# Kernel optimization log

Measured on AMD Instinct MI355X. Metric: run time of the kernel, lower is better.

Reference implementation:

```python
import jax, jax.numpy as jnp
import numpy as np
import math

B, T, Z, H, DOF = 256, 200, 64, 256, 12
NUM_LINKS = 13
POS_DIM = (NUM_LINKS + 1) * 3  # 42
TIME_BANDS = 6
TIME_DIM = 2 * TIME_BANDS + 1  # 13
ACTION_SCALE = 0.25
TRACK_ALPHA = 1.0
SIGMA_MIN, SIGMA_MAX = 0.05, 0.5


def setup_inputs() -> dict:
    key = jax.random.key(0)
    ks = iter(jax.random.split(key, 32))
    rn = lambda shape, s=0.1: jax.random.normal(next(ks), shape, jnp.float32) * s
    inp = {
        'z': jax.random.normal(next(ks), (B, Z), jnp.float32),
        'W_hz': rn((H, Z)), 'b_hz': rn((H,)),
        'W_cz': rn((H, Z)), 'b_cz': rn((H,)),
        'Wih': rn((4 * H, DOF + Z + TIME_DIM)), 'Whh': rn((4 * H, H)),
        'bih': rn((4 * H,)), 'bhh': rn((4 * H,)),
        'Wp1': rn((H, H)), 'bp1': rn((H,)),
        'Wp2': rn((DOF, H)), 'bp2': rn((DOF,)),
        'Wo1': rn((H, H)), 'bo1': rn((H,)),
        'Wo2': rn((3, H)), 'bo2': rn((3,)),
        'Wv': rn((POS_DIM, H)), 'bv': rn((POS_DIM,)),
        'Wfk': rn((NUM_LINKS * 3, DOF)), 'bfk': rn((NUM_LINKS * 3,)),
        'pos_mean': jax.random.normal(next(ks), (NUM_LINKS + 1, 3), jnp.float32),
        'pos_std': 0.5 + jax.random.uniform(next(ks), (NUM_LINKS + 1, 3), jnp.float32),
        'joint_lower': -jnp.ones((DOF,), jnp.float32),
        'joint_upper': jnp.ones((DOF,), jnp.float32),
        'default_dof_pos': jnp.zeros((DOF,), jnp.float32),
    }
    return inp


def _time_features():
    t = jnp.linspace(0.0, 1.0, T)
    feats = [t]
    for k in range(TIME_BANDS):
        f = 2.0 ** k
        feats.append(jnp.sin(2 * math.pi * f * t))
        feats.append(jnp.cos(2 * math.pi * f * t))
    return jnp.stack(feats, axis=-1)  # [T, TIME_DIM]


def reference(z, W_hz, b_hz, W_cz, b_cz, Wih, Whh, bih, bhh,
              Wp1, bp1, Wp2, bp2, Wo1, bo1, Wo2, bo2, Wv, bv, Wfk, bfk,
              pos_mean, pos_std, joint_lower, joint_upper, default_dof_pos):
    joint_range = (joint_upper - joint_lower) / 2.0
    joint_mean = (joint_upper + joint_lower) / 2.0
    time_feats = _time_features()  # [T, TIME_DIM]

    h0 = z @ W_hz.T + b_hz  # [B,H]
    c0 = z @ W_cz.T + b_cz
    prev0 = jnp.broadcast_to(default_dof_pos, (B, DOF))

    def step(carry, tf):
        h, c, prev = carry
        prev_norm = (prev - joint_mean) / joint_range
        x = jnp.concatenate([prev_norm, z, jnp.broadcast_to(tf, (B, TIME_DIM))], axis=-1)
        g = x @ Wih.T + bih + h @ Whh.T + bhh  # [B,4H]
        i, f, gg, o = jnp.split(g, 4, axis=-1)
        c_new = jax.nn.sigmoid(f) * c + jax.nn.sigmoid(i) * jnp.tanh(gg)
        h_new = jax.nn.sigmoid(o) * jnp.tanh(c_new)
        action = jnp.tanh(jax.nn.relu(h_new @ Wp1.T + bp1) @ Wp2.T + bp2)
        target = action * ACTION_SCALE + default_dof_pos
        cur = prev + TRACK_ALPHA * (target - prev)
        clamped = jnp.clip(cur, joint_lower, joint_upper)
        cur_in = cur + jax.lax.stop_gradient(clamped - cur)  # straight-through clamp
        obj = jax.nn.relu(h_new @ Wo1.T + bo1) @ Wo2.T + bo2
        return (h_new, c_new, jax.lax.stop_gradient(cur_in)), (h_new, action, cur, obj)

    _, (H_seq, actions, joints, objs) = jax.lax.scan(step, (h0, c0, prev0), time_feats)
    # [T,B,*] -> [B,T,*]
    H_seq = jnp.swapaxes(H_seq, 0, 1)
    actions_seq = jnp.swapaxes(actions, 0, 1)
    joint_traj = jnp.swapaxes(joints, 0, 1)
    object_traj = jnp.swapaxes(objs, 0, 1)

    agent_traj = joint_traj @ Wfk.T + bfk  # FK: [B,T,39]
    combined = jnp.concatenate([agent_traj, object_traj], axis=-1)  # [B,T,42]
    combined_rs = combined.reshape(B, T, NUM_LINKS + 1, 3)
    graph_x_mu = ((combined_rs - pos_mean) / pos_std).reshape(B, T, POS_DIM)

    sigma = SIGMA_MIN + (SIGMA_MAX - SIGMA_MIN) * jax.nn.sigmoid(H_seq @ Wv.T + bv)
    log_sigma_pos = jnp.log(sigma)
    return (graph_x_mu, joint_traj, actions_seq, log_sigma_pos)
```

## Files before the change

### kernel.cpp

```cpp
#include <hip/hip_runtime.h>
#include <math.h>

#define B_ 256
#define T_ 200
#define H_ 256
#define DOF_ 12

typedef __bf16 bf16;
typedef __bf16 bf16x8 __attribute__((ext_vector_type(8)));
typedef float f32x4 __attribute__((ext_vector_type(4)));

#define XK 288
#define XPAD 296
#define P1PAD 264

#define PI_D 3.14159265358979323846

#define OFF_TF     0u
#define OFF_TCONP  10400u
#define OFF_ZCP    829600u
#define OFF_H0     1878176u
#define OFF_C0     2140320u
#define OFF_WCOMB  2402464u
#define OFF_WP1    2992288u
#define OFF_WP2    3123360u
#define OFF_WO1    3131552u
#define OFF_WO2    3262624u
#define OFF_WV     3270816u
#define OFF_FLAGS  (OFF_WV + 21504u)
#define OFF_HX     3295392u
#define OFF_HSEQ   3558400u

__device__ __forceinline__ float sigf(float x) { return 1.f / (1.f + __expf(-x)); }
__device__ __forceinline__ float tanh_f(float x) {
  float a = fabsf(x);
  float e = __expf(-2.f * a);
  float t = (1.f - e) / (1.f + e);
  return x < 0.f ? -t : t;
}

#define LBAR() asm volatile("s_waitcnt lgkmcnt(0)\n\ts_barrier" ::: "memory")

__global__ void k_zflags(unsigned int* flags) {
  int i = threadIdx.x;
  if (i < 256)
    __hip_atomic_store(&flags[i], 0u, __ATOMIC_RELAXED, __HIP_MEMORY_SCOPE_AGENT);
}

__global__ void k_tfeat(float* tf) {
  int i = blockIdx.x * blockDim.x + threadIdx.x;
  if (i >= T_ * 13) return;
  int t = i / 13, j = i % 13;
  float tv = (float)t / 199.f;
  float v;
  if (j == 0) v = tv;
  else {
    int k = (j - 1) >> 1;
    float f = (float)(1 << k);
    double arg = 2.0 * PI_D * (double)f * (double)tv;
    v = (j & 1) ? (float)sin(arg) : (float)cos(arg);
  }
  tf[i] = v;
}

__global__ void k_prep(const float* __restrict__ tf, const float* __restrict__ Wih,
                       const float* __restrict__ z,
                       const float* __restrict__ bih, const float* __restrict__ bhh,
                       const float* __restrict__ Whz, const float* __restrict__ bhz,
                       const float* __restrict__ Wcz, const float* __restrict__ bcz,
                       float* tconp, float* zcp, float* h0, float* c0) {
  int i = blockIdx.x * blockDim.x + threadIdx.x;
  if (i < 204800) {
    int g = i & 3, q = i >> 2;
    int m = q & 127, hm = (q >> 7) & 1, t = q >> 8;
    int n = g * 256 + 128 * hm + m;
    float s = 0.f;
    #pragma unroll
    for (int j = 0; j < 13; ++j) s += tf[t * 13 + j] * Wih[n * 89 + 76 + j];
    tconp[i] = s;
    return;
  }
  i -= 204800;
  if (i < 262144) {
    int r = i & 3, g = (i >> 2) & 3, tid = (i >> 4) & 511;
    int half = (i >> 13) & 1, pairk = i >> 14;
    int wv = tid >> 6, lr = tid & 15, lq = (tid >> 4) & 3;
    int b = pairk * 16 + lq * 4 + r;
    int n = g * 256 + 128 * half + 16 * wv + lr;
    float s = bih[n] + bhh[n];
    for (int k = 0; k < 64; ++k) s += z[b * 64 + k] * Wih[n * 89 + 12 + k];
    zcp[i] = s;
    return;
  }
  i -= 262144;
  if (i < 65536) {
    int b = i / 256, u = i % 256;
    float s = bhz[u];
    for (int k = 0; k < 64; ++k) s += z[b * 64 + k] * Whz[u * 64 + k];
    h0[i] = s;
    return;
  }
  i -= 65536;
  if (i < 65536) {
    int b = i / 256, u = i % 256;
    float s = bcz[u];
    for (int k = 0; k < 64; ++k) s += z[b * 64 + k] * Wcz[u * 64 + k];
    c0[i] = s;
  }
}

__global__ void k_cast(const float* __restrict__ Whh, const float* __restrict__ Wih,
                       const float* __restrict__ Wp1, const float* __restrict__ Wp2,
                       const float* __restrict__ Wo1, const float* __restrict__ Wo2,
                       const float* __restrict__ Wv,
                       bf16* Wcomb, bf16* Wp1b, bf16* Wp2b, bf16* Wo1b,
                       bf16* Wo2b, bf16* Wvb) {
  int i = blockIdx.x * blockDim.x + threadIdx.x;
  if (i < 294912) {
    int n = i / XK, k = i % XK;
    float v = (k < 256) ? Whh[n * 256 + k]
            : ((k < 268) ? Wih[n * 89 + (k - 256)] : 0.f);
    Wcomb[i] = (bf16)v;
    return;
  }
  i -= 294912;
  if (i < 65536) { Wp1b[i] = (bf16)Wp1[i]; return; }
  i -= 65536;
  if (i < 4096) { int r = i / 256; Wp2b[i] = (bf16)((r < 12) ? Wp2[i] : 0.f); return; }
  i -= 4096;
  if (i < 65536) { Wo1b[i] = (bf16)Wo1[i]; return; }
  i -= 65536;
  if (i < 4096) { int r = i / 256; Wo2b[i] = (bf16)((r < 3) ? Wo2[i] : 0.f); return; }
  i -= 4096;
  if (i < 12288) { int r = i / 256; Wvb[i] = (bf16)((r < 42) ? Wv[i] : 0.f); }
}

__global__ __launch_bounds__(512)
__attribute__((amdgpu_waves_per_eu(2, 2))) void k_recur(
    const float* __restrict__ zcp, const float* __restrict__ tconp,
    const float* __restrict__ h0, const float* __restrict__ c0,
    const bf16* __restrict__ Wcomb, const bf16* __restrict__ Wp1b,
    const bf16* __restrict__ Wp2b,
    const float* __restrict__ bp1, const float* __restrict__ bp2,
    const float* __restrict__ jlo, const float* __restrict__ jhi,
    const float* __restrict__ ddp,
    unsigned long long* hx, unsigned int* flags,
    bf16* __restrict__ Hseq, float* __restrict__ outJ, float* __restrict__ outA) {
  __shared__ bf16 xbuf[16][XPAD];
  __shared__ bf16 w1[272][P1PAD];
  __shared__ bf16 p1buf[16][P1PAD];
  const int tid = threadIdx.x;
  const int wv = tid >> 6, ln = tid & 63, lr = ln & 15, lq = ln >> 4;
  const int bid = blockIdx.x;
  const int pairk = ((bid >> 4) << 3) | (bid & 7);
  const int half = (bid >> 3) & 1;
  const int lbid = pairk * 2 + half;
  const int pbid = bid ^ 8;
  const int b0 = pairk * 16;
  const int u_loc = 16 * wv + lr;
  const int u_gl = 128 * half + u_loc;

  for (int i = tid; i < 272 * 32; i += 512) {
    int r = i >> 5, c8 = (i & 31) * 8;
    bf16x8 v = (r < 256)
      ? *reinterpret_cast<const bf16x8*>(&Wp1b[r * 256 + c8])
      : *reinterpret_cast<const bf16x8*>(&Wp2b[(r - 256) * 256 + c8]);
    *reinterpret_cast<bf16x8*>(&w1[r][c8]) = v;
  }
  for (int i = tid; i < 16 * XPAD; i += 512) {
    int r = i / XPAD, c = i % XPAD;
    float v = 0.f;
    if (c < 256) v = h0[(b0 + r) * 256 + c];
    else if (c < 268) {
      int d = c - 256;
      float lo = jlo[d], hi = jhi[d];
      v = (ddp[d] - 0.5f * (hi + lo)) / (0.5f * (hi - lo));
    }
    xbuf[r][c] = (bf16)v;
  }

  bf16x8 wc[4][9];
  #pragma unroll
  for (int g = 0; g < 4; ++g)
    #pragma unroll
    for (int kt = 0; kt < 9; ++kt) {
      wc[g][kt] = *reinterpret_cast<const bf16x8*>(
          &Wcomb[(size_t)(g * 256 + u_gl) * XK + kt * 32 + lq * 8]);
      f32x4 tmp = __builtin_bit_cast(f32x4, wc[g][kt]);
      asm volatile("" : "+v"(tmp));
      wc[g][kt] = __builtin_bit_cast(bf16x8, tmp);
    }

  float c_reg[4];
  #pragma unroll
  for (int r = 0; r < 4; ++r) c_reg[r] = c0[(b0 + lq * 4 + r) * 256 + u_gl];
  f32x4 zcreg[4];
  #pragma unroll
  for (int g = 0; g < 4; ++g)
    zcreg[g] = *reinterpret_cast<const f32x4*>(
        zcp + ((size_t)lbid * 512 + tid) * 16 + g * 4);
  const float* tcb = tconp + (size_t)(half * 512 + u_loc * 4);
  const float bp1r0 = bp1[32 * wv + lr];
  const float bp1r1 = bp1[32 * wv + 16 + lr];
  float bp2r = 0.f, ddr = 0.f, lor = -1.f, hir = 1.f;
  if (lr < 12) { bp2r = bp2[lr]; ddr = ddp[lr]; lor = jlo[lr]; hir = jhi[lr]; }
  const float jmr = 0.5f * (hir + lor), jrr = 0.5f * (hir - lor);
  bf16* hs = Hseq + ((size_t)(b0 + lq * 4) * T_) * 256 + u_gl;

  unsigned int* myf = &flags[bid * 8 + wv];
  unsigned int* pf  = &flags[pbid * 8 + wv];
  const int wru = 16 * wv + (ln >> 2), wrc = ln & 3;
  const int rcol = 128 * (half ^ 1) + wru;
  unsigned long long* hxw0 = &hx[(((size_t)(pairk * 2 + 0) * 2 + half) * 128 + u_loc) * 4 + lq];
  unsigned long long* hxw1 = &hx[(((size_t)(pairk * 2 + 1) * 2 + half) * 128 + u_loc) * 4 + lq];
  unsigned long long* hxr0 = &hx[(((size_t)(pairk * 2 + 0) * 2 + (half ^ 1)) * 128 + wru) * 4 + wrc];
  unsigned long long* hxr1 = &hx[(((size_t)(pairk * 2 + 1) * 2 + (half ^ 1)) * 128 + wru) * 4 + wrc];

  f32x4 tcv = *reinterpret_cast<const f32x4*>(tcb);
  __syncthreads();
  bool dead = false;

  for (int t = 0; t < T_; ++t) {
    f32x4 ac[4];
    #pragma unroll
    for (int g = 0; g < 4; ++g) ac[g] = zcreg[g] + tcv[g];
    #pragma unroll
    for (int kt = 0; kt < 9; ++kt) {
      bf16x8 a = *reinterpret_cast<const bf16x8*>(&xbuf[lr][kt * 32 + lq * 8]);
      #pragma unroll
      for (int g = 0; g < 4; ++g)
        ac[g] = __builtin_amdgcn_mfma_f32_16x16x32_bf16(a, wc[g][kt], ac[g], 0, 0, 0);
    }
    LBAR();

    union { unsigned long long v; unsigned short s[4]; } pk;
    bf16 hb4[4];
    #pragma unroll
    for (int r = 0; r < 4; ++r) {
      float cn = sigf(ac[1][r]) * c_reg[r] + sigf(ac[0][r]) * tanh_f(ac[2][r]);
      float hn = sigf(ac[3][r]) * tanh_f(cn);
      c_reg[r] = cn;
      bf16 hb = (bf16)hn;
      hb4[r] = hb;
      xbuf[lq * 4 + r][u_gl] = hb;
      pk.s[r] = __builtin_bit_cast(unsigned short, hb);
    }
    __hip_atomic_store((t & 1) ? hxw1 : hxw0, pk.v,
                       __ATOMIC_RELAXED, __HIP_MEMORY_SCOPE_AGENT);
    asm volatile("s_waitcnt vmcnt(0)" ::: "memory");
    const unsigned int want = t + 1;
    if (ln == 0)
      __hip_atomic_store(myf, want, __ATOMIC_RELAXED, __HIP_MEMORY_SCOPE_AGENT);
    #pragma unroll
    for (int r = 0; r < 4; ++r)
      hs[(size_t)r * (T_ * 256) + (size_t)t * 256] = hb4[r];
    f32x4 tcn = *reinterpret_cast<const f32x4*>(
        tcb + (size_t)((t + 1 < T_) ? t + 1 : t) * 1024);

    if (!dead) {
      int guard = 1 << 18;
      for (;;) {
        unsigned int fv =
            __hip_atomic_load(pf, __ATOMIC_RELAXED, __HIP_MEMORY_SCOPE_AGENT);
        if ((int)(fv - want) >= 0) break;
        if (--guard == 0) { dead = true; break; }
      }
    }
    unsigned long long pv = __hip_atomic_load((t & 1) ? hxr1 : hxr0,
                                              __ATOMIC_RELAXED,
                                              __HIP_MEMORY_SCOPE_AGENT);
    {
      unsigned short* ph = (unsigned short*)&pv;
      #pragma unroll
      for (int j = 0; j < 4; ++j)
        xbuf[wrc * 4 + j][rcol] = __builtin_bit_cast(bf16, ph[j]);
    }
    LBAR();

    {
      f32x4 acc0 = {bp1r0, bp1r0, bp1r0, bp1r0};
      f32x4 acc1 = {bp1r1, bp1r1, bp1r1, bp1r1};
      #pragma unroll
      for (int kt = 0; kt < 8; ++kt) {
        bf16x8 av = *reinterpret_cast<const bf16x8*>(&xbuf[lr][kt * 32 + lq * 8]);
        bf16x8 b0v = *reinterpret_cast<const bf16x8*>(&w1[32 * wv + lr][kt * 32 + lq * 8]);
        bf16x8 b1v = *reinterpret_cast<const bf16x8*>(&w1[32 * wv + 16 + lr][kt * 32 + lq * 8]);
        acc0 = __builtin_amdgcn_mfma_f32_16x16x32_bf16(av, b0v, acc0, 0, 0, 0);
        acc1 = __builtin_amdgcn_mfma_f32_16x16x32_bf16(av, b1v, acc1, 0, 0, 0);
      }
      #pragma unroll
      for (int r = 0; r < 4; ++r) {
        p1buf[lq * 4 + r][32 * wv + lr] = (bf16)fmaxf(acc0[r], 0.f);
        p1buf[lq * 4 + r][32 * wv + 16 + lr] = (bf16)fmaxf(acc1[r], 0.f);
      }
    }
    LBAR();

    if (wv == 0) {
      f32x4 acc = {0.f, 0.f, 0.f, 0.f};
      #pragma unroll
      for (int kt = 0; kt < 8; ++kt) {
        bf16x8 ap = *reinterpret_cast<const bf16x8*>(&p1buf[lr][kt * 32 + lq * 8]);
        bf16x8 w2 = *reinterpret_cast<const bf16x8*>(&w1[256 + lr][kt * 32 + lq * 8]);
        acc = __builtin_amdgcn_mfma_f32_16x16x32_bf16(ap, w2, acc, 0, 0, 0);
      }
      if (lr < 12) {
        #pragma unroll
        for (int r = 0; r < 4; ++r) {
          int b = lq * 4 + r;
          float act = tanh_f(acc[r] + bp2r);
          float curp = act * 0.25f + ddr;
          float cl = fminf(fmaxf(curp, lor), hir);
          if (half == 0) {
            size_t o = ((size_t)(b0 + b) * T_ + t) * 12 + lr;
            outA[o] = act;
            outJ[o] = curp;
          }
          xbuf[b][256 + lr] = (bf16)((cl - jmr) / jrr);
        }
      }
    }
    LBAR();
    tcv = tcn;
  }
}

__global__ __launch_bounds__(256) void k_post(
    const bf16* __restrict__ Hseq, const bf16* __restrict__ Wo1b,
    const bf16* __restrict__ Wo2b, const bf16* __restrict__ Wvb,
    const float* __restrict__ bo1, const float* __restrict__ bo2,
    const float* __restrict__ bv,
    const float* __restrict__ Wfk, const float* __restrict__ bfk,
    const float* __restrict__ pm, const float* __restrict__ ps,
    const float* __restrict__ joints, float* __restrict__ out0,
    float* __restrict__ out3) {
  __shared__ bf16 u1buf[16][P1PAD];
  __shared__ float objbuf[16][3];
  __shared__ float jbuf[16][12];
  const int tid = threadIdx.x;
  const int wv = tid >> 6;
  const int ln = tid & 63;
  const int lr = ln & 15;
  const int lq = ln >> 4;

  bf16x8 wo1f[4][8];
  float bo1r[4];
  #pragma unroll
  for (int jn = 0; jn < 4; ++jn) {
    int n0 = wv * 64 + jn * 16;
    bo1r[jn] = bo1[n0 + lr];
    #pragma unroll
    for (int kt = 0; kt < 8; ++kt)
      wo1f[jn][kt] = *reinterpret_cast<const bf16x8*>(
          &Wo1b[(size_t)(n0 + lr) * 256 + kt * 32 + lq * 8]);
  }
  const int col = (wv - 1) * 16 + lr;
  bf16x8 wvf[8];
  float bvr = 0.f;
  if (wv >= 1) {
    #pragma unroll
    for (int kt = 0; kt < 8; ++kt)
      wvf[kt] = *reinterpret_cast<const bf16x8*>(
          &Wvb[(size_t)col * 256 + kt * 32 + lq * 8]);
    bvr = (col < 42) ? bv[col] : 0.f;
  }
  bf16x8 wo2f[8];
  if (wv == 0) {
    #pragma unroll
    for (int kt = 0; kt < 8; ++kt)
      wo2f[kt] = *reinterpret_cast<const bf16x8*>(
          &Wo2b[(size_t)lr * 256 + kt * 32 + lq * 8]);
  }

  for (int it = 0; it < 10; ++it) {
    int tt = blockIdx.x * 10 + it;
    size_t r0 = (size_t)tt * 16;
    bf16x8 ah[8];
    #pragma unroll
    for (int kt = 0; kt < 8; ++kt)
      ah[kt] = *reinterpret_cast<const bf16x8*>(&Hseq[(r0 + lr) * 256 + kt * 32 + lq * 8]);
    #pragma unroll
    for (int jn = 0; jn < 4; ++jn) {
      int n0 = wv * 64 + jn * 16;
      float bb = bo1r[jn];
      f32x4 acc = {bb, bb, bb, bb};
      #pragma unroll
      for (int kt = 0; kt < 8; ++kt)
        acc = __builtin_amdgcn_mfma_f32_16x16x32_bf16(ah[kt], wo1f[jn][kt], acc, 0, 0, 0);
      #pragma unroll
      for (int r = 0; r < 4; ++r)
        u1buf[lq * 4 + r][n0 + lr] = (bf16)fmaxf(acc[r], 0.f);
    }
    if (wv >= 1) {
      f32x4 acc = {bvr, bvr, bvr, bvr};
      #pragma unroll
      for (int kt = 0; kt < 8; ++kt)
        acc = __builtin_amdgcn_mfma_f32_16x16x32_bf16(ah[kt], wvf[kt], acc, 0, 0, 0);
      if (col < 42) {
        #pragma unroll
        for (int r = 0; r < 4; ++r) {
          float s = 0.05f + 0.45f * sigf(acc[r]);
          out3[(r0 + lq * 4 + r) * 42 + col] = __logf(s);
        }
      }
    }
    if (tid < 192) {
      int rr = tid / 12, d = tid % 12;
      jbuf[rr][d] = joints[(r0 + rr) * 12 + d];
    }
    __syncthreads();
    if (wv == 0) {
      bf16x8 ap[8];
      #pragma unroll
      for (int kt = 0; kt < 8; ++kt)
        ap[kt] = *reinterpret_cast<const bf16x8*>(&u1buf[lr][kt * 32 + lq * 8]);
      f32x4 acc = {0.f, 0.f, 0.f, 0.f};
      #pragma unroll
      for (int kt = 0; kt < 8; ++kt)
        acc = __builtin_amdgcn_mfma_f32_16x16x32_bf16(ap[kt], wo2f[kt], acc, 0, 0, 0);
      if (lr < 3) {
        #pragma unroll
        for (int r = 0; r < 4; ++r)
          objbuf[lq * 4 + r][lr] = acc[r] + bo2[lr];
      }
    }
    __syncthreads();
    for (int e = tid; e < 16 * 42; e += 256) {
      int rr = e / 42, pd = e % 42;
      float v;
      if (pd < 39) {
        float s = bfk[pd];
        #pragma unroll
        for (int d = 0; d < 12; ++d) s += jbuf[rr][d] * Wfk[pd * 12 + d];
        v = s;
      } else v = objbuf[rr][pd - 39];
      out0[(r0 + rr) * 42 + pd] = (v - pm[pd]) / ps[pd];
    }
    __syncthreads();
  }
}

extern "C" void kernel_launch(void* const* d_in, const int* in_sizes, int n_in,
                              void* d_out, int out_size, void* d_ws, size_t ws_size,
                              hipStream_t stream) {
  const float* z   = (const float*)d_in[0];
  const float* Whz = (const float*)d_in[1];
  const float* bhz = (const float*)d_in[2];
  const float* Wcz = (const float*)d_in[3];
  const float* bcz = (const float*)d_in[4];
  const float* Wih = (const float*)d_in[5];
  const float* Whh = (const float*)d_in[6];
  const float* bih = (const float*)d_in[7];
  const float* bhh = (const float*)d_in[8];
  const float* Wp1 = (const float*)d_in[9];
  const float* bp1 = (const float*)d_in[10];
  const float* Wp2 = (const float*)d_in[11];
  const float* bp2 = (const float*)d_in[12];
  const float* Wo1 = (const float*)d_in[13];
  const float* bo1 = (const float*)d_in[14];
  const float* Wo2 = (const float*)d_in[15];
  const float* bo2 = (const float*)d_in[16];
  const float* Wv  = (const float*)d_in[17];
  const float* bv  = (const float*)d_in[18];
  const float* Wfk = (const float*)d_in[19];
  const float* bfk = (const float*)d_in[20];
  const float* pm  = (const float*)d_in[21];
  const float* ps  = (const float*)d_in[22];
  const float* jlo = (const float*)d_in[23];
  const float* jhi = (const float*)d_in[24];
  const float* ddp = (const float*)d_in[25];

  char* ws = (char*)d_ws;
  float* tf    = (float*)(ws + OFF_TF);
  float* tconp = (float*)(ws + OFF_TCONP);
  float* zcp   = (float*)(ws + OFF_ZCP);
  float* h0    = (float*)(ws + OFF_H0);
  float* c0    = (float*)(ws + OFF_C0);
  bf16* Wcomb  = (bf16*)(ws + OFF_WCOMB);
  bf16* Wp1b   = (bf16*)(ws + OFF_WP1);
  bf16* Wp2b   = (bf16*)(ws + OFF_WP2);
  bf16* Wo1b   = (bf16*)(ws + OFF_WO1);
  bf16* Wo2b   = (bf16*)(ws + OFF_WO2);
  bf16* Wvb    = (bf16*)(ws + OFF_WV);
  unsigned long long* hx = (unsigned long long*)(ws + OFF_HX);
  unsigned int* flags    = (unsigned int*)(ws + OFF_FLAGS);
  bf16* Hseq   = (bf16*)(ws + OFF_HSEQ);

  float* out  = (float*)d_out;
  float* out0 = out;
  float* outJ = out + 2150400;
  float* outA = out + 2764800;
  float* out3 = out + 3379200;

  k_zflags<<<1, 256, 0, stream>>>(flags);
  k_tfeat<<<11, 256, 0, stream>>>(tf);
  k_prep<<<2336, 256, 0, stream>>>(tf, Wih, z, bih, bhh, Whz, bhz, Wcz, bcz,
                                   tconp, zcp, h0, c0);
  k_cast<<<1744, 256, 0, stream>>>(Whh, Wih, Wp1, Wp2, Wo1, Wo2, Wv,
                                   Wcomb, Wp1b, Wp2b, Wo1b, Wo2b, Wvb);
  k_recur<<<32, 512, 0, stream>>>(zcp, tconp, h0, c0, Wcomb, Wp1b, Wp2b,
                                  bp1, bp2, jlo, jhi, ddp, hx, flags,
                                  Hseq, outJ, outA);
  k_post<<<320, 256, 0, stream>>>(Hseq, Wo1b, Wo2b, Wvb, bo1, bo2, bv,
                                  Wfk, bfk, pm, ps, outJ, out0, out3);
}
```

Baseline: 1.122 ms.

## Replace flag-based cross-block handoff with sequence-tagged hidden-state packets

New measurement: 1.119 ms. Within noise of the previous version (-0.3%).

```diff
diff --git a/kernel.cpp b/kernel.cpp
--- a/kernel.cpp
+++ b/kernel.cpp
@@ -9,6 +9,7 @@
 typedef __bf16 bf16;
 typedef __bf16 bf16x8 __attribute__((ext_vector_type(8)));
 typedef float f32x4 __attribute__((ext_vector_type(4)));
+typedef unsigned long long u64;
 
 #define XK 288
 #define XPAD 296
@@ -27,9 +28,8 @@
 #define OFF_WO1    3131552u
 #define OFF_WO2    3262624u
 #define OFF_WV     3270816u
-#define OFF_FLAGS  (OFF_WV + 21504u)
 #define OFF_HX     3295392u
-#define OFF_HSEQ   3558400u
+#define OFF_HSEQ   3819680u
 
 __device__ __forceinline__ float sigf(float x) { return 1.f / (1.f + __expf(-x)); }
 __device__ __forceinline__ float tanh_f(float x) {
@@ -40,12 +40,6 @@
 }
 
 #define LBAR() asm volatile("s_waitcnt lgkmcnt(0)\n\ts_barrier" ::: "memory")
-
-__global__ void k_zflags(unsigned int* flags) {
-  int i = threadIdx.x;
-  if (i < 256)
-    __hip_atomic_store(&flags[i], 0u, __ATOMIC_RELAXED, __HIP_MEMORY_SCOPE_AGENT);
-}
 
 __global__ void k_tfeat(float* tf) {
   int i = blockIdx.x * blockDim.x + threadIdx.x;
@@ -135,8 +129,7 @@
   if (i < 12288) { int r = i / 256; Wvb[i] = (bf16)((r < 42) ? Wv[i] : 0.f); }
 }
 
-__global__ __launch_bounds__(512)
-__attribute__((amdgpu_waves_per_eu(2, 2))) void k_recur(
+__global__ __launch_bounds__(512, 2) void k_recur(
     const float* __restrict__ zcp, const float* __restrict__ tconp,
     const float* __restrict__ h0, const float* __restrict__ c0,
     const bf16* __restrict__ Wcomb, const bf16* __restrict__ Wp1b,
@@ -144,7 +137,7 @@
     const float* __restrict__ bp1, const float* __restrict__ bp2,
     const float* __restrict__ jlo, const float* __restrict__ jhi,
     const float* __restrict__ ddp,
-    unsigned long long* hx, unsigned int* flags,
+    u64* hxt,
     bf16* __restrict__ Hseq, float* __restrict__ outJ, float* __restrict__ outA) {
   __shared__ bf16 xbuf[16][XPAD];
   __shared__ bf16 w1[272][P1PAD];
@@ -155,7 +148,6 @@
   const int pairk = ((bid >> 4) << 3) | (bid & 7);
   const int half = (bid >> 3) & 1;
   const int lbid = pairk * 2 + half;
-  const int pbid = bid ^ 8;
   const int b0 = pairk * 16;
   const int u_loc = 16 * wv + lr;
   const int u_gl = 128 * half + u_loc;
@@ -179,17 +171,15 @@
     xbuf[r][c] = (bf16)v;
   }
 
-  bf16x8 wc[4][9];
+  f32x4 wc0[9], wc1[9], wc2[9], wc3[9];
   #pragma unroll
-  for (int g = 0; g < 4; ++g)
-    #pragma unroll
-    for (int kt = 0; kt < 9; ++kt) {
-      wc[g][kt] = *reinterpret_cast<const bf16x8*>(
-          &Wcomb[(size_t)(g * 256 + u_gl) * XK + kt * 32 + lq * 8]);
-      f32x4 tmp = __builtin_bit_cast(f32x4, wc[g][kt]);
-      asm volatile("" : "+v"(tmp));
-      wc[g][kt] = __builtin_bit_cast(bf16x8, tmp);
-    }
+  for (int kt = 0; kt < 9; ++kt) {
+    wc0[kt] = *reinterpret_cast<const f32x4*>(&Wcomb[(size_t)(0 * 256 + u_gl) * XK + kt * 32 + lq * 8]);
+    wc1[kt] = *reinterpret_cast<const f32x4*>(&Wcomb[(size_t)(1 * 256 + u_gl) * XK + kt * 32 + lq * 8]);
+    wc2[kt] = *reinterpret_cast<const f32x4*>(&Wcomb[(size_t)(2 * 256 + u_gl) * XK + kt * 32 + lq * 8]);
+    wc3[kt] = *reinterpret_cast<const f32x4*>(&Wcomb[(size_t)(3 * 256 + u_gl) * XK + kt * 32 + lq * 8]);
+    asm volatile("" : "+a"(wc0[kt]), "+a"(wc1[kt]), "+a"(wc2[kt]), "+a"(wc3[kt]));
+  }
 
   float c_reg[4];
   #pragma unroll
@@ -207,14 +197,12 @@
   const float jmr = 0.5f * (hir + lor), jrr = 0.5f * (hir - lor);
   bf16* hs = Hseq + ((size_t)(b0 + lq * 4) * T_) * 256 + u_gl;
 
-  unsigned int* myf = &flags[bid * 8 + wv];
-  unsigned int* pf  = &flags[pbid * 8 + wv];
   const int wru = 16 * wv + (ln >> 2), wrc = ln & 3;
   const int rcol = 128 * (half ^ 1) + wru;
-  unsigned long long* hxw0 = &hx[(((size_t)(pairk * 2 + 0) * 2 + half) * 128 + u_loc) * 4 + lq];
-  unsigned long long* hxw1 = &hx[(((size_t)(pairk * 2 + 1) * 2 + half) * 128 + u_loc) * 4 + lq];
-  unsigned long long* hxr0 = &hx[(((size_t)(pairk * 2 + 0) * 2 + (half ^ 1)) * 128 + wru) * 4 + wrc];
-  unsigned long long* hxr1 = &hx[(((size_t)(pairk * 2 + 1) * 2 + (half ^ 1)) * 128 + wru) * 4 + wrc];
+  u64* pws0 = hxt + ((((size_t)(pairk * 2 + 0) * 2 + half) * 128 + u_loc) * 4 + lq) * 2;
+  u64* pws1 = hxt + ((((size_t)(pairk * 2 + 1) * 2 + half) * 128 + u_loc) * 4 + lq) * 2;
+  u64* prs0 = hxt + ((((size_t)(pairk * 2 + 0) * 2 + (half ^ 1)) * 128 + wru) * 4 + wrc) * 2;
+  u64* prs1 = hxt + ((((size_t)(pairk * 2 + 1) * 2 + (half ^ 1)) * 128 + wru) * 4 + wrc) * 2;
 
   f32x4 tcv = *reinterpret_cast<const f32x4*>(tcb);
   __syncthreads();
@@ -227,13 +215,15 @@
     #pragma unroll
     for (int kt = 0; kt < 9; ++kt) {
       bf16x8 a = *reinterpret_cast<const bf16x8*>(&xbuf[lr][kt * 32 + lq * 8]);
-      #pragma unroll
-      for (int g = 0; g < 4; ++g)
-        ac[g] = __builtin_amdgcn_mfma_f32_16x16x32_bf16(a, wc[g][kt], ac[g], 0, 0, 0);
+      asm volatile("" : "+a"(wc0[kt]), "+a"(wc1[kt]), "+a"(wc2[kt]), "+a"(wc3[kt]));
+      ac[0] = __builtin_amdgcn_mfma_f32_16x16x32_bf16(a, __builtin_bit_cast(bf16x8, wc0[kt]), ac[0], 0, 0, 0);
+      ac[1] = __builtin_amdgcn_mfma_f32_16x16x32_bf16(a, __builtin_bit_cast(bf16x8, wc1[kt]), ac[1], 0, 0, 0);
+      ac[2] = __builtin_amdgcn_mfma_f32_16x16x32_bf16(a, __builtin_bit_cast(bf16x8, wc2[kt]), ac[2], 0, 0, 0);
+      ac[3] = __builtin_amdgcn_mfma_f32_16x16x32_bf16(a, __builtin_bit_cast(bf16x8, wc3[kt]), ac[3], 0, 0, 0);
     }
     LBAR();
 
-    union { unsigned long long v; unsigned short s[4]; } pk;
+    union { u64 v[1]; unsigned short s[4]; } pk;
     bf16 hb4[4];
     #pragma unroll
     for (int r = 0; r < 4; ++r) {
@@ -242,39 +232,40 @@
       c_reg[r] = cn;
       bf16 hb = (bf16)hn;
       hb4[r] = hb;
-      xbuf[lq * 4 + r][u_gl] = hb;
       pk.s[r] = __builtin_bit_cast(unsigned short, hb);
     }
-    __hip_atomic_store((t & 1) ? hxw1 : hxw0, pk.v,
-                       __ATOMIC_RELAXED, __HIP_MEMORY_SCOPE_AGENT);
-    asm volatile("s_waitcnt vmcnt(0)" ::: "memory");
     const unsigned int want = t + 1;
-    if (ln == 0)
-      __hip_atomic_store(myf, want, __ATOMIC_RELAXED, __HIP_MEMORY_SCOPE_AGENT);
-    #pragma unroll
-    for (int r = 0; r < 4; ++r)
+    {
+      u64 q0 = ((u64)want << 32) | (u64)pk.s[0] | ((u64)pk.s[1] << 16);
+      u64 q1 = ((u64)want << 32) | (u64)pk.s[2] | ((u64)pk.s[3] << 16);
+      u64* pw = (t & 1) ? pws1 : pws0;
+      __hip_atomic_store(pw, q0, __ATOMIC_RELAXED, __HIP_MEMORY_SCOPE_AGENT);
+      __hip_atomic_store(pw + 1, q1, __ATOMIC_RELAXED, __HIP_MEMORY_SCOPE_AGENT);
+    }
+    #pragma unroll
+    for (int r = 0; r < 4; ++r) {
+      xbuf[lq * 4 + r][u_gl] = hb4[r];
       hs[(size_t)r * (T_ * 256) + (size_t)t * 256] = hb4[r];
+    }
     f32x4 tcn = *reinterpret_cast<const f32x4*>(
         tcb + (size_t)((t + 1 < T_) ? t + 1 : t) * 1024);
 
-    if (!dead) {
-      int guard = 1 << 18;
+    u64 pq0, pq1;
+    {
+      u64* pr = (t & 1) ? prs1 : prs0;
+      int guard = 1 << 16;
       for (;;) {
-        unsigned int fv =
-            __hip_atomic_load(pf, __ATOMIC_RELAXED, __HIP_MEMORY_SCOPE_AGENT);
-        if ((int)(fv - want) >= 0) break;
-        if (--guard == 0) { dead = true; break; }
-      }
-    }
-    unsigned long long pv = __hip_atomic_load((t & 1) ? hxr1 : hxr0,
-                                              __ATOMIC_RELAXED,
-                                              __HIP_MEMORY_SCOPE_AGENT);
-    {
-      unsigned short* ph = (unsigned short*)&pv;
-      #pragma unroll
-      for (int j = 0; j < 4; ++j)
-        xbuf[wrc * 4 + j][rcol] = __builtin_bit_cast(bf16, ph[j]);
-    }
+        pq0 = __hip_atomic_load(pr, __ATOMIC_RELAXED, __HIP_MEMORY_SCOPE_AGENT);
+        pq1 = __hip_atomic_load(pr + 1, __ATOMIC_RELAXED, __HIP_MEMORY_SCOPE_AGENT);
+        int ok = ((unsigned)(pq0 >> 32) == want) & ((unsigned)(pq1 >> 32) == want);
+        if (__all(ok)) break;
+        if (dead || --guard == 0) { dead = true; break; }
+      }
+    }
+    xbuf[wrc * 4 + 0][rcol] = __builtin_bit_cast(bf16, (unsigned short)(pq0));
+    xbuf[wrc * 4 + 1][rcol] = __builtin_bit_cast(bf16, (unsigned short)(pq0 >> 16));
+    xbuf[wrc * 4 + 2][rcol] = __builtin_bit_cast(bf16, (unsigned short)(pq1));
+    xbuf[wrc * 4 + 3][rcol] = __builtin_bit_cast(bf16, (unsigned short)(pq1 >> 16));
     LBAR();
 
     {
@@ -482,8 +473,7 @@
   bf16* Wo1b   = (bf16*)(ws + OFF_WO1);
   bf16* Wo2b   = (bf16*)(ws + OFF_WO2);
   bf16* Wvb    = (bf16*)(ws + OFF_WV);
-  unsigned long long* hx = (unsigned long long*)(ws + OFF_HX);
-  unsigned int* flags    = (unsigned int*)(ws + OFF_FLAGS);
+  u64* hxt     = (u64*)(ws + OFF_HX);
   bf16* Hseq   = (bf16*)(ws + OFF_HSEQ);
 
   float* out  = (float*)d_out;
@@ -492,14 +482,13 @@
   float* outA = out + 2764800;
   float* out3 = out + 3379200;
 
-  k_zflags<<<1, 256, 0, stream>>>(flags);
   k_tfeat<<<11, 256, 0, stream>>>(tf);
   k_prep<<<2336, 256, 0, stream>>>(tf, Wih, z, bih, bhh, Whz, bhz, Wcz, bcz,
                                    tconp, zcp, h0, c0);
   k_cast<<<1744, 256, 0, stream>>>(Whh, Wih, Wp1, Wp2, Wo1, Wo2, Wv,
                                    Wcomb, Wp1b, Wp2b, Wo1b, Wo2b, Wvb);
   k_recur<<<32, 512, 0, stream>>>(zcp, tconp, h0, c0, Wcomb, Wp1b, Wp2b,
-                                  bp1, bp2, jlo, jhi, ddp, hx, flags,
+                                  bp1, bp2, jlo, jhi, ddp, hxt,
                                   Hseq, outJ, outA);
   k_post<<<320, 256, 0, stream>>>(Hseq, Wo1b, Wo2b, Wvb, bo1, bo2, bv,
                                   Wfk, bfk, pm, ps, outJ, out0, out3);
```
